# Optimization experiments

Measured on AMD Instinct MI355X. Metric: run time of the kernel, lower is better.

Reference implementation:

```python
import jax, jax.numpy as jnp
import numpy as np

DIM = 1024
HEADS = 16
HEAD_DIM = DIM // HEADS
B, N = 2, 2048


def setup_inputs() -> dict:
    key = jax.random.key(0)
    k1, k2, k3, k4 = jax.random.split(key, 4)
    scale = 1.0 / np.sqrt(DIM)
    return {
        "x": jax.random.normal(k1, (B, N, DIM), dtype=jnp.float32),
        "w_qkv": jax.random.normal(k2, (DIM, 3 * DIM), dtype=jnp.float32) * scale,
        "w_out": jax.random.normal(k3, (DIM, DIM), dtype=jnp.float32) * scale,
        "b_out": jax.random.normal(k4, (DIM,), dtype=jnp.float32) * 0.01,
    }


def reference(x, w_qkv, w_out, b_out):
    b, n, c = x.shape
    h, d = HEADS, c // HEADS
    sm_scale = d ** -0.5
    qkv = x @ w_qkv  # [b, n, 3c]
    q, k, v = jnp.split(qkv, 3, axis=-1)
    # [b, n, c] -> [b, h, n, d]
    q = q.reshape(b, n, h, d).transpose(0, 2, 1, 3)
    k = k.reshape(b, n, h, d).transpose(0, 2, 1, 3)
    v = v.reshape(b, n, h, d).transpose(0, 2, 1, 3)
    dots = jnp.einsum("bhqd,bhkd->bhqk", q, k) * sm_scale
    attn = jax.nn.softmax(dots, axis=-1)
    out = jnp.einsum("bhqk,bhkd->bhqd", attn, v)
    out = out.transpose(0, 2, 1, 3).reshape(b, n, c)
    return out @ w_out + b_out
```

## Files before the change

### kernel.cpp

```cpp
#include <hip/hip_runtime.h>
#include <hip/hip_bf16.h>

typedef __attribute__((ext_vector_type(8))) short bf16x8;
typedef __attribute__((ext_vector_type(4))) float f32x4;

#define B_    2
#define N_    2048
#define DIM_  1024
#define H_    16
#define D_    64
#define BH_   32
#define QSC   0.18033688f

static __device__ __forceinline__ void gload_lds16(const void* g, void* l) {
  __builtin_amdgcn_global_load_lds((const __attribute__((address_space(1))) void*)g,
                                   (__attribute__((address_space(3))) void*)l, 16, 0, 0);
}

__global__ __launch_bounds__(256) void prep_kernel(const float* __restrict__ x,
                                                   const float* __restrict__ w_qkv,
                                                   const float* __restrict__ w_out,
                                                   __hip_bfloat16* __restrict__ xb,
                                                   __hip_bfloat16* __restrict__ wqkT,
                                                   __hip_bfloat16* __restrict__ woT) {
  __shared__ float tile[64][65];
  const int bid = blockIdx.x, t = threadIdx.x;
  if (bid < 4096) {
    const int i = bid * 256 + t;
    float4 v = reinterpret_cast<const float4*>(x)[i];
    union { __hip_bfloat16 h[4]; uint2 u; } cv;
    cv.h[0] = __float2bfloat16(v.x);
    cv.h[1] = __float2bfloat16(v.y);
    cv.h[2] = __float2bfloat16(v.z);
    cv.h[3] = __float2bfloat16(v.w);
    reinterpret_cast<uint2*>(xb)[i] = cv.u;
    return;
  }
  const float* in;
  __hip_bfloat16* out;
  int R, C, c0, r0;
  if (bid < 4096 + 768) {
    const int bx = bid - 4096;
    in = w_qkv; out = wqkT; R = 1024; C = 3072;
    c0 = (bx % 48) * 64; r0 = (bx / 48) * 64;
  } else {
    const int bx = bid - 4096 - 768;
    in = w_out; out = woT; R = 1024; C = 1024;
    c0 = (bx % 16) * 64; r0 = (bx / 16) * 64;
  }
#pragma unroll
  for (int i = 0; i < 16; ++i) {
    int idx = i * 256 + t;
    int r = idx >> 6, c = idx & 63;
    tile[r][c] = in[(size_t)(r0 + r) * C + (c0 + c)];
  }
  __syncthreads();
#pragma unroll
  for (int i = 0; i < 16; ++i) {
    int idx = i * 256 + t;
    int rr = idx >> 6, cc = idx & 63;
    out[(size_t)(c0 + rr) * R + (r0 + cc)] = __float2bfloat16(tile[cc][rr]);
  }
}

__global__ __launch_bounds__(512, 2) void gemm_qkv_kernel(const __hip_bfloat16* __restrict__ A,
                                                          const __hip_bfloat16* __restrict__ Bt,
                                                          __hip_bfloat16* __restrict__ Qw,
                                                          __hip_bfloat16* __restrict__ Kw,
                                                          __hip_bfloat16* __restrict__ Vt) {
  __shared__ __align__(16) char lds[131072];
  const int t = threadIdx.x, w = t >> 6, lane = t & 63;
  const int l16 = lane & 15, kg = lane >> 4;
  int flat = blockIdx.y * 12 + blockIdx.x;
  flat = (flat & 7) * 24 + (flat >> 3);
  const int bx = flat % 12, by = flat / 12;
  const int m0 = by * 256, n0 = bx * 256;
  const int wm = w >> 2, wn = w & 3;
  const int rA = t >> 3;
  const int jb = (t & 7) ^ (rA & 7);

#define LDSOFF(bb, mat) (((bb) * 2 + (mat)) * 32768)
#define STG_A(bb, tt, h)                                                                    \
  do {                                                                                      \
    gload_lds16(A + (size_t)(m0 + rA + 64 * (h)) * 1024 + (tt) * 64 + jb * 8,               \
                (char*)lds + LDSOFF(bb, 0) + (h) * 8192 + t * 16);                          \
    gload_lds16(A + (size_t)(m0 + rA + 64 * (h) + 128) * 1024 + (tt) * 64 + jb * 8,         \
                (char*)lds + LDSOFF(bb, 0) + (h) * 8192 + 16384 + t * 16);                  \
  } while (0)
#define STG_B(bb, tt, h)                                                                    \
  do {                                                                                      \
    gload_lds16(Bt + (size_t)(n0 + rA + 128 * (h)) * 1024 + (tt) * 64 + jb * 8,             \
                (char*)lds + LDSOFF(bb, 1) + (h) * 16384 + t * 16);                         \
    gload_lds16(Bt + (size_t)(n0 + rA + 128 * (h) + 64) * 1024 + (tt) * 64 + jb * 8,        \
                (char*)lds + LDSOFF(bb, 1) + (h) * 16384 + 8192 + t * 16);                  \
  } while (0)
#define RD_A(dst, q, i, kk)                                                                 \
  {                                                                                         \
    const int row = wm * 128 + ((q) * 2 + (i)) * 16 + l16;                                  \
    dst = *reinterpret_cast<const bf16x8*>(Ab + row * 128 + ((((kk) * 4 + kg) ^ (row & 7)) * 16)); \
  }
#define RD_B(dst, nj, kk)                                                                   \
  {                                                                                         \
    const int row = wn * 64 + (nj) * 16 + l16;                                              \
    dst = *reinterpret_cast<const bf16x8*>(Bb + row * 128 + ((((kk) * 4 + kg) ^ (row & 7)) * 16)); \
  }
#define PHASE(q)                                                                            \
  do {                                                                                      \
    bf16x8 af[2][2];                                                                        \
    _Pragma("unroll") for (int i = 0; i < 2; ++i)                                           \
      _Pragma("unroll") for (int kk = 0; kk < 2; ++kk) RD_A(af[i][kk], q, i, kk);           \
    __builtin_amdgcn_s_setprio(1);                                                          \
    _Pragma("unroll") for (int i = 0; i < 2; ++i)                                           \
      _Pragma("unroll") for (int nj = 0; nj < 4; ++nj)                                      \
        _Pragma("unroll") for (int kk = 0; kk < 2; ++kk)                                    \
          acc[(q) * 2 + i][nj] =                                                            \
              __builtin_amdgcn_mfma_f32_16x16x32_bf16(af[i][kk], bfr[nj][kk],               \
                                                      acc[(q) * 2 + i][nj], 0, 0, 0);       \
    __builtin_amdgcn_s_setprio(0);                                                          \
  } while (0)

  f32x4 acc[8][4];
#pragma unroll
  for (int i = 0; i < 8; ++i)
#pragma unroll
    for (int j = 0; j < 4; ++j) acc[i][j] = {0.f, 0.f, 0.f, 0.f};

  STG_A(0, 0, 0); STG_A(0, 0, 1); STG_B(0, 0, 0); STG_B(0, 0, 1);
  STG_B(1, 1, 0); STG_B(1, 1, 1); STG_A(1, 1, 0);

#pragma unroll 1
  for (int kt = 0; kt < 16; ++kt) {
    const int b = kt & 1;
    const char* Ab = (const char*)lds + LDSOFF(b, 0);
    const char* Bb = (const char*)lds + LDSOFF(b, 1);

    if (kt < 15) STG_A(b ^ 1, kt + 1, 1);
    __builtin_amdgcn_sched_barrier(0);
    if (kt < 15) asm volatile("s_waitcnt vmcnt(8)" ::: "memory");
    else         asm volatile("s_waitcnt vmcnt(0)" ::: "memory");
    __builtin_amdgcn_s_barrier();
    __builtin_amdgcn_sched_barrier(0);
    bf16x8 bfr[4][2];
#pragma unroll
    for (int nj = 0; nj < 4; ++nj)
#pragma unroll
      for (int kk = 0; kk < 2; ++kk) RD_B(bfr[nj][kk], nj, kk);
    PHASE(0);
    __builtin_amdgcn_s_barrier();
    __builtin_amdgcn_sched_barrier(0);

    if (kt < 14) STG_B(b, kt + 2, 0);
    __builtin_amdgcn_sched_barrier(0);
    PHASE(1);
    __builtin_amdgcn_s_barrier();
    __builtin_amdgcn_sched_barrier(0);

    if (kt < 14) STG_B(b, kt + 2, 1);
    PHASE(2);

    if (kt < 14) STG_A(b, kt + 2, 0);
    __builtin_amdgcn_sched_barrier(0);
    PHASE(3);
    __builtin_amdgcn_s_barrier();
    __builtin_amdgcn_sched_barrier(0);
  }

  const int which = n0 >> 10;
#pragma unroll
  for (int nj = 0; nj < 4; ++nj) {
    const int n = n0 + wn * 64 + nj * 16 + l16;
    const int nn = n & 1023;
    const int h = nn >> 6, d = nn & 63;
#pragma unroll
    for (int mi = 0; mi < 8; ++mi) {
      const int m = m0 + wm * 128 + mi * 16 + kg * 4;
      const int bb = m >> 11, tt = m & 2047;
      if (which == 2) {
        union { __hip_bfloat16 hh[4]; unsigned long long u; } pv;
#pragma unroll
        for (int r = 0; r < 4; ++r) pv.hh[r] = __float2bfloat16(acc[mi][nj][r]);
        *reinterpret_cast<unsigned long long*>(
            &Vt[((size_t)(bb * H_ + h) * D_ + d) * N_ + tt]) = pv.u;
      } else {
        __hip_bfloat16* dst = (which == 0) ? Qw : Kw;
        const float sc = (which == 0) ? QSC : 1.0f;
#pragma unroll
        for (int r = 0; r < 4; ++r)
          dst[((size_t)(bb * H_ + h) * N_ + tt + r) * D_ + d] = __float2bfloat16(acc[mi][nj][r] * sc);
      }
    }
  }
#undef PHASE
#undef RD_B
#undef RD_A
#undef STG_B
#undef STG_A
#undef LDSOFF
}

__global__ __launch_bounds__(256) void gemm_out_kernel(const __hip_bfloat16* __restrict__ A,
                                                       const __hip_bfloat16* __restrict__ Bt,
                                                       const float* __restrict__ bo,
                                                       float* __restrict__ out) {
  __shared__ __align__(16) char lds[65536];
  const int t = threadIdx.x, w = t >> 6, lane = t & 63;
  const int l16 = lane & 15, kg = lane >> 4;
  const int m0 = blockIdx.y * 128, n0 = blockIdx.x * 128;
  const int wm = w >> 1, wn = w & 1;

  f32x4 acc[4][4];
#pragma unroll
  for (int i = 0; i < 4; ++i)
#pragma unroll
    for (int j = 0; j < 4; ++j) acc[i][j] = {0.f, 0.f, 0.f, 0.f};

  size_t srcA[4], srcB[4];
#pragma unroll
  for (int i = 0; i < 4; ++i) {
    const int c = 256 * i + t;
    const int row = c >> 3, jsw = (c & 7) ^ (row & 7);
    srcA[i] = (size_t)(m0 + row) * 1024 + jsw * 8;
    srcB[i] = (size_t)(n0 + row) * 1024 + jsw * 8;
  }
#define OSTG(bb, k0)                                                          \
  do {                                                                        \
    _Pragma("unroll") for (int i = 0; i < 4; ++i) {                           \
      gload_lds16(A + srcA[i] + (k0), (char*)lds + (bb) * 32768 + i * 4096 + w * 1024);          \
      gload_lds16(Bt + srcB[i] + (k0), (char*)lds + (bb) * 32768 + 16384 + i * 4096 + w * 1024); \
    }                                                                         \
  } while (0)

  OSTG(0, 0);

#pragma unroll 1
  for (int kt = 0; kt < 16; ++kt) {
    const int b = kt & 1;
    __builtin_amdgcn_s_barrier();
    __builtin_amdgcn_sched_barrier(0);
    if (kt + 1 < 16) OSTG(b ^ 1, (kt + 1) * 64);
    __builtin_amdgcn_sched_barrier(0);
    if (kt + 1 < 16) asm volatile("s_waitcnt vmcnt(8)" ::: "memory");
    else             asm volatile("s_waitcnt vmcnt(0)" ::: "memory");
    __builtin_amdgcn_s_barrier();
    __builtin_amdgcn_sched_barrier(0);
    const char* Ab = (const char*)lds + b * 32768;
    const char* Bb = (const char*)lds + b * 32768 + 16384;
#pragma unroll
    for (int kk = 0; kk < 2; ++kk) {
      bf16x8 a[4], bfr[4];
#pragma unroll
      for (int i = 0; i < 4; ++i) {
        const int row = wm * 64 + i * 16 + l16;
        const int jsw = ((kk << 2) | kg) ^ (row & 7);
        a[i] = *reinterpret_cast<const bf16x8*>(Ab + row * 128 + jsw * 16);
      }
#pragma unroll
      for (int j = 0; j < 4; ++j) {
        const int row = wn * 64 + j * 16 + l16;
        const int jsw = ((kk << 2) | kg) ^ (row & 7);
        bfr[j] = *reinterpret_cast<const bf16x8*>(Bb + row * 128 + jsw * 16);
      }
      __builtin_amdgcn_s_setprio(1);
#pragma unroll
      for (int i = 0; i < 4; ++i)
#pragma unroll
        for (int j = 0; j < 4; ++j)
          acc[i][j] = __builtin_amdgcn_mfma_f32_16x16x32_bf16(a[i], bfr[j], acc[i][j], 0, 0, 0);
      __builtin_amdgcn_s_setprio(0);
    }
  }
#undef OSTG

#pragma unroll
  for (int j = 0; j < 4; ++j) {
    const int n = n0 + wn * 64 + j * 16 + l16;
    const float bias = bo[n];
#pragma unroll
    for (int i = 0; i < 4; ++i) {
#pragma unroll
      for (int r = 0; r < 4; ++r) {
        const int m = m0 + wm * 64 + i * 16 + kg * 4 + r;
        out[(size_t)m * 1024 + n] = acc[i][j][r] + bias;
      }
    }
  }
}

__global__ __launch_bounds__(512) void attn_kernel(const __hip_bfloat16* __restrict__ Q,
                                                   const __hip_bfloat16* __restrict__ K,
                                                   const __hip_bfloat16* __restrict__ Vt,
                                                   __hip_bfloat16* __restrict__ O) {
  __shared__ __align__(16) __hip_bfloat16 Ks[3][64 * 64];
  __shared__ __align__(16) __hip_bfloat16 Vs[3][64 * 64];
  __shared__ __align__(16) __hip_bfloat16 Plds[8][16][64];
  const int bh = blockIdx.y;
  const int q0 = blockIdx.x * 128;
  const int t = threadIdx.x, w = t >> 6, lane = t & 63;
  const int l16 = lane & 15, kg = lane >> 4;
  const int b = bh >> 4, h = bh & 15;

  const __hip_bfloat16* Kbh = K + (size_t)bh * N_ * D_;
  const __hip_bfloat16* Vbh = Vt + (size_t)bh * D_ * N_;

  const int crow = t >> 3, cb = t & 7;
  const int csw = cb ^ (crow & 7);
  const size_t offK = (size_t)crow * D_ + csw * 8;
  const size_t offV = (size_t)crow * N_ + csw * 8;

  const __hip_bfloat16* Qp = Q + ((size_t)bh * N_ + q0 + w * 16 + l16) * D_ + kg * 8;
  const bf16x8 qf0 = *reinterpret_cast<const bf16x8*>(Qp);
  const bf16x8 qf1 = *reinterpret_cast<const bf16x8*>(Qp + 32);

  float dacc = 0.f;
  f32x4 oacc[4];
#pragma unroll
  for (int dn = 0; dn < 4; ++dn) oacc[dn] = {0.f, 0.f, 0.f, 0.f};

#define STAGE(bufi, kv)                                                          \
  do {                                                                           \
    gload_lds16(Kbh + (size_t)(kv) * D_ + offK, (char*)Ks[bufi] + w * 1024);     \
    gload_lds16(Vbh + (kv) + offV,              (char*)Vs[bufi] + w * 1024);     \
  } while (0)

  STAGE(0, 0);
  STAGE(1, 64);

#pragma unroll 1
  for (int it = 0; it < N_ / 64; ++it) {
    if (it < N_ / 64 - 1) asm volatile("s_waitcnt vmcnt(2)" ::: "memory");
    else                  asm volatile("s_waitcnt vmcnt(0)" ::: "memory");
    __builtin_amdgcn_s_barrier();
    __builtin_amdgcn_sched_barrier(0);
    if (it + 2 < N_ / 64) STAGE((it + 2) % 3, (it + 2) * 64);
    __builtin_amdgcn_sched_barrier(0);

    const char* Kb = (const char*)Ks[it % 3];
    const char* Vb = (const char*)Vs[it % 3];

    f32x4 s[4];
#pragma unroll
    for (int kt = 0; kt < 4; ++kt) s[kt] = {0.f, 0.f, 0.f, 0.f};
    __builtin_amdgcn_s_setprio(1);
#pragma unroll
    for (int kt = 0; kt < 4; ++kt) {
      const int row = kt * 16 + l16;
      const int rsw = (row & 7) << 4;
      const bf16x8 k0 = *reinterpret_cast<const bf16x8*>(Kb + row * 128 + ((kg << 4) ^ rsw));
      const bf16x8 k1 = *reinterpret_cast<const bf16x8*>(Kb + row * 128 + (((4 + kg) << 4) ^ rsw));
      s[kt] = __builtin_amdgcn_mfma_f32_16x16x32_bf16(k0, qf0, s[kt], 0, 0, 0);
      s[kt] = __builtin_amdgcn_mfma_f32_16x16x32_bf16(k1, qf1, s[kt], 0, 0, 0);
    }
    __builtin_amdgcn_s_setprio(0);

    const int xm3 = (l16 & 7) << 3;
    float ds = 0.f;
#pragma unroll
    for (int kt = 0; kt < 4; ++kt) {
      const float p0 = __builtin_amdgcn_exp2f(s[kt][0]);
      const float p1 = __builtin_amdgcn_exp2f(s[kt][1]);
      const float p2 = __builtin_amdgcn_exp2f(s[kt][2]);
      const float p3 = __builtin_amdgcn_exp2f(s[kt][3]);
      ds += (p0 + p1) + (p2 + p3);
      union { __hip_bfloat162 h2[2]; unsigned long long u; } pk;
      pk.h2[0] = __float22bfloat162_rn(make_float2(p0, p1));
      pk.h2[1] = __float22bfloat162_rn(make_float2(p2, p3));
      *reinterpret_cast<unsigned long long*>(&Plds[w][l16][(16 * kt + 4 * kg) ^ xm3]) = pk.u;
    }
    dacc += ds;

    __builtin_amdgcn_s_setprio(1);
#pragma unroll
    for (int kk = 0; kk < 2; ++kk) {
      const bf16x8 pa = *reinterpret_cast<const bf16x8*>(
          &Plds[w][l16][(kk * 32 + kg * 8) ^ xm3]);
#pragma unroll
      for (int dn = 0; dn < 4; ++dn) {
        const int vrow = dn * 16 + l16;
        const int vsw = (vrow & 7) << 4;
        const bf16x8 vf = *reinterpret_cast<const bf16x8*>(
            Vb + vrow * 128 + ((kk * 64 + kg * 16) ^ vsw));
        oacc[dn] = __builtin_amdgcn_mfma_f32_16x16x32_bf16(pa, vf, oacc[dn], 0, 0, 0);
      }
    }
    __builtin_amdgcn_s_setprio(0);
  }
#undef STAGE

  float dtot = dacc + __shfl_xor(dacc, 16);
  dtot += __shfl_xor(dtot, 32);
  float inv[4];
#pragma unroll
  for (int r = 0; r < 4; ++r) inv[r] = 1.0f / __shfl(dtot, kg * 4 + r);

  __hip_bfloat16* Ob = O + ((size_t)b * N_ + q0 + w * 16) * DIM_ + h * D_;
#pragma unroll
  for (int dn = 0; dn < 4; ++dn)
#pragma unroll
    for (int r = 0; r < 4; ++r)
      Ob[(size_t)(kg * 4 + r) * DIM_ + dn * 16 + l16] = __float2bfloat16(oacc[dn][r] * inv[r]);
}

extern "C" void kernel_launch(void* const* d_in, const int* in_sizes, int n_in,
                              void* d_out, int out_size, void* d_ws, size_t ws_size,
                              hipStream_t stream) {
  const float* x = (const float*)d_in[0];
  const float* w_qkv = (const float*)d_in[1];
  const float* w_out = (const float*)d_in[2];
  const float* b_out = (const float*)d_in[3];
  float* out = (float*)d_out;

  __hip_bfloat16* ws = (__hip_bfloat16*)d_ws;
  __hip_bfloat16* xb = ws;
  __hip_bfloat16* wqkT = xb + (size_t)4096 * 1024;
  __hip_bfloat16* woT = wqkT + (size_t)3072 * 1024;
  __hip_bfloat16* Qw = woT + (size_t)1024 * 1024;
  __hip_bfloat16* Kw = Qw + (size_t)BH_ * N_ * D_;
  __hip_bfloat16* Vt = Kw + (size_t)BH_ * N_ * D_;
  __hip_bfloat16* Ow = Vt + (size_t)BH_ * N_ * D_;

  prep_kernel<<<5120, 256, 0, stream>>>(x, w_qkv, w_out, xb, wqkT, woT);
  gemm_qkv_kernel<<<dim3(12, 16), 512, 0, stream>>>(xb, wqkT, Qw, Kw, Vt);
  attn_kernel<<<dim3(16, 32), 512, 0, stream>>>(Qw, Kw, Vt, Ow);
  gemm_out_kernel<<<dim3(8, 32), 256, 0, stream>>>(Ow, woT, b_out, out);
}
```

Measured before the change: 116.3 us.

## Shrink attention blocks to 256 threads with double buffering and MFMA row sums

The attention kernel now uses 4 waves per block covering 64 queries, launched on twice as many blocks, with a 2-deep K/V LDS ring instead of 3-deep. Each thread issues two 16-byte global-to-LDS loads per tensor, and the wait and barrier move to the end of each iteration. The softmax denominator is now computed with an extra MFMA against a vector of ones, replacing the scalar exp accumulation and cross-lane shuffles. This aims for more resident blocks and less VALU work, but the prefetch distance is shorter and each block now re-reads K/V for fewer queries, doubling K/V traffic.

```diff
diff --git a/kernel.cpp b/kernel.cpp
--- a/kernel.cpp
+++ b/kernel.cpp
@@ -286,15 +286,15 @@
   }
 }
 
-__global__ __launch_bounds__(512) void attn_kernel(const __hip_bfloat16* __restrict__ Q,
-                                                   const __hip_bfloat16* __restrict__ K,
-                                                   const __hip_bfloat16* __restrict__ Vt,
-                                                   __hip_bfloat16* __restrict__ O) {
-  __shared__ __align__(16) __hip_bfloat16 Ks[3][64 * 64];
-  __shared__ __align__(16) __hip_bfloat16 Vs[3][64 * 64];
-  __shared__ __align__(16) __hip_bfloat16 Plds[8][16][64];
+__global__ __launch_bounds__(256, 4) void attn_kernel(const __hip_bfloat16* __restrict__ Q,
+                                                      const __hip_bfloat16* __restrict__ K,
+                                                      const __hip_bfloat16* __restrict__ Vt,
+                                                      __hip_bfloat16* __restrict__ O) {
+  __shared__ __align__(16) __hip_bfloat16 Ks[2][64 * 64];
+  __shared__ __align__(16) __hip_bfloat16 Vs[2][64 * 64];
+  __shared__ __align__(16) __hip_bfloat16 Plds[4][16][64];
   const int bh = blockIdx.y;
-  const int q0 = blockIdx.x * 128;
+  const int q0 = blockIdx.x * 64;
   const int t = threadIdx.x, w = t >> 6, lane = t & 63;
   const int l16 = lane & 15, kg = lane >> 4;
   const int b = bh >> 4, h = bh & 15;
@@ -311,31 +311,34 @@
   const bf16x8 qf0 = *reinterpret_cast<const bf16x8*>(Qp);
   const bf16x8 qf1 = *reinterpret_cast<const bf16x8*>(Qp + 32);
 
-  float dacc = 0.f;
+  bf16x8 ones;
+#pragma unroll
+  for (int i = 0; i < 8; ++i) ones[i] = (short)0x3F80;
+
+  f32x4 oaccS = {0.f, 0.f, 0.f, 0.f};
   f32x4 oacc[4];
 #pragma unroll
   for (int dn = 0; dn < 4; ++dn) oacc[dn] = {0.f, 0.f, 0.f, 0.f};
 
-#define STAGE(bufi, kv)                                                          \
-  do {                                                                           \
-    gload_lds16(Kbh + (size_t)(kv) * D_ + offK, (char*)Ks[bufi] + w * 1024);     \
-    gload_lds16(Vbh + (kv) + offV,              (char*)Vs[bufi] + w * 1024);     \
+#define STAGE(bufi, kv)                                                                   \
+  do {                                                                                    \
+    gload_lds16(Kbh + (size_t)(kv) * D_ + offK,             (char*)Ks[bufi] + t * 16);    \
+    gload_lds16(Kbh + (size_t)(kv) * D_ + offK + 32 * D_,   (char*)Ks[bufi] + 4096 + t * 16); \
+    gload_lds16(Vbh + (kv) + offV,                          (char*)Vs[bufi] + t * 16);    \
+    gload_lds16(Vbh + (kv) + offV + 32 * N_,                (char*)Vs[bufi] + 4096 + t * 16); \
   } while (0)
 
   STAGE(0, 0);
-  STAGE(1, 64);
+  asm volatile("s_waitcnt vmcnt(0)" ::: "memory");
+  __builtin_amdgcn_s_barrier();
 
 #pragma unroll 1
   for (int it = 0; it < N_ / 64; ++it) {
-    if (it < N_ / 64 - 1) asm volatile("s_waitcnt vmcnt(2)" ::: "memory");
-    else                  asm volatile("s_waitcnt vmcnt(0)" ::: "memory");
-    __builtin_amdgcn_s_barrier();
-    __builtin_amdgcn_sched_barrier(0);
-    if (it + 2 < N_ / 64) STAGE((it + 2) % 3, (it + 2) * 64);
-    __builtin_amdgcn_sched_barrier(0);
-
-    const char* Kb = (const char*)Ks[it % 3];
-    const char* Vb = (const char*)Vs[it % 3];
+    const int buf = it & 1;
+    if (it + 1 < N_ / 64) STAGE(buf ^ 1, (it + 1) * 64);
+
+    const char* Kb = (const char*)Ks[buf];
+    const char* Vb = (const char*)Vs[buf];
 
     f32x4 s[4];
 #pragma unroll
@@ -353,26 +356,22 @@
     __builtin_amdgcn_s_setprio(0);
 
     const int xm3 = (l16 & 7) << 3;
-    float ds = 0.f;
 #pragma unroll
     for (int kt = 0; kt < 4; ++kt) {
-      const float p0 = __builtin_amdgcn_exp2f(s[kt][0]);
-      const float p1 = __builtin_amdgcn_exp2f(s[kt][1]);
-      const float p2 = __builtin_amdgcn_exp2f(s[kt][2]);
-      const float p3 = __builtin_amdgcn_exp2f(s[kt][3]);
-      ds += (p0 + p1) + (p2 + p3);
       union { __hip_bfloat162 h2[2]; unsigned long long u; } pk;
-      pk.h2[0] = __float22bfloat162_rn(make_float2(p0, p1));
-      pk.h2[1] = __float22bfloat162_rn(make_float2(p2, p3));
+      pk.h2[0] = __float22bfloat162_rn(make_float2(__builtin_amdgcn_exp2f(s[kt][0]),
+                                                   __builtin_amdgcn_exp2f(s[kt][1])));
+      pk.h2[1] = __float22bfloat162_rn(make_float2(__builtin_amdgcn_exp2f(s[kt][2]),
+                                                   __builtin_amdgcn_exp2f(s[kt][3])));
       *reinterpret_cast<unsigned long long*>(&Plds[w][l16][(16 * kt + 4 * kg) ^ xm3]) = pk.u;
     }
-    dacc += ds;
 
     __builtin_amdgcn_s_setprio(1);
 #pragma unroll
     for (int kk = 0; kk < 2; ++kk) {
       const bf16x8 pa = *reinterpret_cast<const bf16x8*>(
           &Plds[w][l16][(kk * 32 + kg * 8) ^ xm3]);
+      oaccS = __builtin_amdgcn_mfma_f32_16x16x32_bf16(pa, ones, oaccS, 0, 0, 0);
 #pragma unroll
       for (int dn = 0; dn < 4; ++dn) {
         const int vrow = dn * 16 + l16;
@@ -383,15 +382,15 @@
       }
     }
     __builtin_amdgcn_s_setprio(0);
+
+    asm volatile("s_waitcnt vmcnt(0)" ::: "memory");
+    __builtin_amdgcn_s_barrier();
   }
 #undef STAGE
 
-  float dtot = dacc + __shfl_xor(dacc, 16);
-  dtot += __shfl_xor(dtot, 32);
   float inv[4];
 #pragma unroll
-  for (int r = 0; r < 4; ++r) inv[r] = 1.0f / __shfl(dtot, kg * 4 + r);
-
+  for (int r = 0; r < 4; ++r) inv[r] = 1.0f / oaccS[r];
   __hip_bfloat16* Ob = O + ((size_t)b * N_ + q0 + w * 16) * DIM_ + h * D_;
 #pragma unroll
   for (int dn = 0; dn < 4; ++dn)
@@ -420,6 +419,6 @@
 
   prep_kernel<<<5120, 256, 0, stream>>>(x, w_qkv, w_out, xb, wqkT, woT);
   gemm_qkv_kernel<<<dim3(12, 16), 512, 0, stream>>>(xb, wqkT, Qw, Kw, Vt);
-  attn_kernel<<<dim3(16, 32), 512, 0, stream>>>(Qw, Kw, Vt, Ow);
+  attn_kernel<<<dim3(32, 32), 256, 0, stream>>>(Qw, Kw, Vt, Ow);
   gemm_out_kernel<<<dim3(8, 32), 256, 0, stream>>>(Ow, woT, b_out, out);
 }
```

Measured after the change: 118.9 us. 2.3% more time.
